# Kernel tuning notes

Measured on AMD Instinct MI355X. Metric: run time of the kernel, lower is better.

The kernel has to match this reference:

```python
import jax, jax.numpy as jnp
import numpy as np

N = 20000   # nodes
E = 320000  # edges
F = 64      # input node features
H = 256     # hidden_layer_size
C = 10      # nbr_classes
G = 64      # graphs in the batch


def _lin(key, fan_in, fan_out):
    k1, k2 = jax.random.split(key)
    bound = 1.0 / np.sqrt(fan_in)
    W = jax.random.uniform(k1, (fan_in, fan_out), jnp.float32, -bound, bound)
    b = jax.random.uniform(k2, (fan_out,), jnp.float32, -bound, bound)
    return W, b


def setup_inputs() -> dict:
    key = jax.random.key(0)
    ks = jax.random.split(key, 10)
    x = jax.random.normal(ks[0], (N, F), jnp.float32)
    edge_index = jax.random.randint(ks[1], (2, E), 0, N)
    batch = jnp.sort(jax.random.randint(ks[2], (N,), 0, G))
    W1, b1 = _lin(ks[3], F, H)
    W2, b2 = _lin(ks[4], H, H)
    W3, b3 = _lin(ks[5], H, H)
    W4, b4 = _lin(ks[6], H, H)
    W5, b5 = _lin(ks[7], H, H)
    Wout, bout = _lin(ks[8], H, C)
    return {"x": x, "edge_index": edge_index, "batch": batch,
            "W1": W1, "b1": b1, "W2": W2, "b2": b2, "W3": W3, "b3": b3,
            "W4": W4, "b4": b4, "W5": W5, "b5": b5, "Wout": Wout, "bout": bout}


def reference(x, edge_index, batch, W1, b1, W2, b2, W3, b3, W4, b4, W5, b5, Wout, bout):
    # GCNConv (Kipf & Welling): add self-loops, D^{-1/2}(A+I)D^{-1/2} (X W) + b.
    # Dropout(p=0.5) is identity in eval mode (reference is deterministic).
    loop = jnp.arange(N)
    row = jnp.concatenate([edge_index[0], loop])  # source nodes, [E+N]
    col = jnp.concatenate([edge_index[1], loop])  # target nodes, [E+N]
    deg = jax.ops.segment_sum(jnp.ones(E + N, x.dtype), col, num_segments=N)
    dinv = jax.lax.rsqrt(deg)  # deg >= 1 thanks to self-loops
    norm = (dinv[row] * dinv[col])[:, None]  # [E+N, 1]

    def gcn_conv(h, W, b):
        m = (h @ W)[row] * norm                      # gather + normalize, [E+N, H]
        return jax.ops.segment_sum(m, col, num_segments=N) + b

    h = x
    for W, b in ((W1, b1), (W2, b2), (W3, b3), (W4, b4), (W5, b5)):
        h = jax.nn.relu(gcn_conv(h, W, b))

    # global_mean_pool over graph ids
    counts = jax.ops.segment_sum(jnp.ones(N, h.dtype), batch, num_segments=G)
    pooled = jax.ops.segment_sum(h, batch, num_segments=G) / jnp.maximum(counts, 1.0)[:, None]
    return pooled @ Wout + bout  # [G, C]
```

## Files before the change

### kernel.cpp

```cpp
#include <hip/hip_runtime.h>

#define NN 20000
#define NE 320000
#define FIN 64
#define HD 256
#define NC 10
#define NG 64
#define NB ((NN + 255) / 256)

typedef unsigned short u16;
typedef unsigned int u32;
typedef __attribute__((ext_vector_type(8))) short short8;
typedef __attribute__((ext_vector_type(4))) float f32x4;

__device__ __forceinline__ float bf2f(u16 u) {
    union { u32 i; float f; } v; v.i = ((u32)u) << 16; return v.f;
}
__device__ __forceinline__ u16 f2bf(float f) {
    union { float f; u32 i; } v; v.f = f;
    u32 r = v.i + 0x7fffu + ((v.i >> 16) & 1u);
    return (u16)(r >> 16);
}

__global__ void k_prep(int* __restrict__ degi, int* __restrict__ gstart) {
    int i = blockIdx.x * 256 + threadIdx.x;
    if (i < NN) degi[i] = 0;
    if (i < NG) gstart[i] = NN;
}

__global__ void k_deg(const int* __restrict__ col, int* __restrict__ degi,
                      const int* __restrict__ batch, int* __restrict__ gstart) {
    int i = blockIdx.x * 256 + threadIdx.x;
    if (i < NE) atomicAdd(&degi[col[i]], 1);
    if (i < NN) {
        int b = batch[i];
        int prev = (i == 0) ? -1 : batch[i - 1];
        if (b != prev) gstart[b] = i;
    }
}

__global__ __launch_bounds__(256) void k_scan1(const int* __restrict__ degi,
                                               int* __restrict__ rowptr,
                                               int* __restrict__ bsum) {
    int t = threadIdx.x;
    int i = blockIdx.x * 256 + t;
    int v = (i < NN) ? degi[i] : 0;
    int lane = t & 63, wid = t >> 6;
    int x = v;
#pragma unroll
    for (int off = 1; off < 64; off <<= 1) {
        int y = __shfl_up(x, off);
        if (lane >= off) x += y;
    }
    __shared__ int ws[4];
    if (lane == 63) ws[wid] = x;
    __syncthreads();
    int woff = 0;
    for (int w = 0; w < wid; ++w) woff += ws[w];
    if (i < NN) rowptr[i] = woff + x - v;
    if (t == 255) bsum[blockIdx.x] = woff + x;
}

__global__ __launch_bounds__(128) void k_scan2(int* __restrict__ bsum, int* __restrict__ rowptr) {
    __shared__ int s[NB + 1];
    int t = threadIdx.x;
    if (t < NB) s[t] = bsum[t];
    __syncthreads();
    if (t == 0) {
        int run = 0;
        for (int k = 0; k < NB; ++k) { int tmp = s[k]; s[k] = run; run += tmp; }
        s[NB] = run;
    }
    __syncthreads();
    if (t < NB) bsum[t] = s[t];
    if (t == 0) rowptr[NN] = s[NB];
}

__global__ void k_scan3(const int* __restrict__ degi, const int* __restrict__ bsum,
                        int* __restrict__ rowptr, int* __restrict__ cursor,
                        float* __restrict__ dinv,
                        const float* __restrict__ x, u16* __restrict__ u0) {
    int i = blockIdx.x * 256 + threadIdx.x;
    if (i < NN) {
        int rp = rowptr[i] + bsum[i >> 8];
        rowptr[i] = rp;
        cursor[i] = rp;
        dinv[i] = rsqrtf((float)(1 + degi[i]));
    }
    if (i < NN * FIN / 4) {
        int node = i >> 4;
        float d = rsqrtf((float)(1 + degi[node]));
        float4 v = *(const float4*)&x[(size_t)i * 4];
        u32 lo = (u32)f2bf(v.x * d) | ((u32)f2bf(v.y * d) << 16);
        u32 hi = (u32)f2bf(v.z * d) | ((u32)f2bf(v.w * d) << 16);
        *(uint2*)&u0[(size_t)i * 4] = make_uint2(lo, hi);
    }
}

__global__ void k_fill(const int* __restrict__ row, const int* __restrict__ col,
                       int* __restrict__ cursor, int* __restrict__ ebuf) {
    int e = blockIdx.x * 256 + threadIdx.x;
    if (e < NE) {
        int c = col[e];
        int pos = atomicAdd(&cursor[c], 1);
        ebuf[pos] = row[e];
    }
}

__global__ __launch_bounds__(256) void k_trans(const float* __restrict__ W0, const float* __restrict__ W1,
                                               const float* __restrict__ W2, const float* __restrict__ W3,
                                               const float* __restrict__ W4,
                                               u16* __restrict__ T0, u16* __restrict__ T1,
                                               u16* __restrict__ T2, u16* __restrict__ T3,
                                               u16* __restrict__ T4) {
    int l = blockIdx.z;
    const float* W = (l == 0) ? W0 : (l == 1) ? W1 : (l == 2) ? W2 : (l == 3) ? W3 : W4;
    u16* T = (l == 0) ? T0 : (l == 1) ? T1 : (l == 2) ? T2 : (l == 3) ? T3 : T4;
    int K = (l == 0) ? FIN : HD;
    int k0 = blockIdx.x * 32;
    if (k0 >= K) return;
    int n0 = blockIdx.y * 32;
    __shared__ float tile[32][33];
    int tx = threadIdx.x & 31, ty = threadIdx.x >> 5;
#pragma unroll
    for (int r = 0; r < 32; r += 8)
        tile[ty + r][tx] = W[(size_t)(k0 + ty + r) * HD + n0 + tx];
    __syncthreads();
#pragma unroll
    for (int r = 0; r < 32; r += 8)
        T[(size_t)(n0 + ty + r) * K + k0 + tx] = f2bf(tile[tx][ty + r]);
}

__global__ __launch_bounds__(256) void k_gather256(const u16* __restrict__ U,
                                                   const int* __restrict__ rowptr,
                                                   const int* __restrict__ ebuf,
                                                   const float* __restrict__ dinv,
                                                   u16* __restrict__ Z) {
    int n = blockIdx.x * 4 + (threadIdx.x >> 6);
    if (n >= NN) return;
    int lane = threadIdx.x & 63;
    int half = lane >> 5;
    int seg = lane & 31;
    int s = rowptr[n], e = rowptr[n + 1];
    float acc[8];
    if (half == 0) {
        uint4 v = *(const uint4*)&U[(size_t)n * HD + seg * 8];
        acc[0] = bf2f((u16)(v.x & 0xffff)); acc[1] = bf2f((u16)(v.x >> 16));
        acc[2] = bf2f((u16)(v.y & 0xffff)); acc[3] = bf2f((u16)(v.y >> 16));
        acc[4] = bf2f((u16)(v.z & 0xffff)); acc[5] = bf2f((u16)(v.z >> 16));
        acc[6] = bf2f((u16)(v.w & 0xffff)); acc[7] = bf2f((u16)(v.w >> 16));
    } else {
#pragma unroll
        for (int k = 0; k < 8; ++k) acc[k] = 0.f;
    }
    for (int j = s; j < e; j += 32) {
        int idx = j + lane;
        int myid = (lane < 32 && idx < e) ? ebuf[idx] : -1;
        uint4 v[16];
#pragma unroll
        for (int k = 0; k < 16; ++k) {
            int r = __shfl(myid, 2 * k + half);
            uint4 t = *(const uint4*)&U[(size_t)max(r, 0) * HD + seg * 8];
            if (r < 0) t = make_uint4(0u, 0u, 0u, 0u);
            v[k] = t;
        }
#pragma unroll
        for (int k = 0; k < 16; ++k) {
            acc[0] += bf2f((u16)(v[k].x & 0xffff)); acc[1] += bf2f((u16)(v[k].x >> 16));
            acc[2] += bf2f((u16)(v[k].y & 0xffff)); acc[3] += bf2f((u16)(v[k].y >> 16));
            acc[4] += bf2f((u16)(v[k].z & 0xffff)); acc[5] += bf2f((u16)(v[k].z >> 16));
            acc[6] += bf2f((u16)(v[k].w & 0xffff)); acc[7] += bf2f((u16)(v[k].w >> 16));
        }
    }
#pragma unroll
    for (int k = 0; k < 8; ++k) acc[k] += __shfl_xor(acc[k], 32);
    if (half == 0) {
        float d = dinv[n];
        uint4 o;
        o.x = (u32)f2bf(acc[0] * d) | ((u32)f2bf(acc[1] * d) << 16);
        o.y = (u32)f2bf(acc[2] * d) | ((u32)f2bf(acc[3] * d) << 16);
        o.z = (u32)f2bf(acc[4] * d) | ((u32)f2bf(acc[5] * d) << 16);
        o.w = (u32)f2bf(acc[6] * d) | ((u32)f2bf(acc[7] * d) << 16);
        *(uint4*)&Z[(size_t)n * HD + seg * 8] = o;
    }
}

__global__ __launch_bounds__(256) void k_gather64(const u16* __restrict__ U,
                                                  const int* __restrict__ rowptr,
                                                  const int* __restrict__ ebuf,
                                                  const float* __restrict__ dinv,
                                                  u16* __restrict__ Z) {
    int n = blockIdx.x * 4 + (threadIdx.x >> 6);
    if (n >= NN) return;
    int lane = threadIdx.x & 63;
    int grp = lane >> 3;
    int seg = lane & 7;
    int s = rowptr[n], e = rowptr[n + 1];
    float acc[8];
    if (grp == 0) {
        uint4 v = *(const uint4*)&U[(size_t)n * FIN + seg * 8];
        acc[0] = bf2f((u16)(v.x & 0xffff)); acc[1] = bf2f((u16)(v.x >> 16));
        acc[2] = bf2f((u16)(v.y & 0xffff)); acc[3] = bf2f((u16)(v.y >> 16));
        acc[4] = bf2f((u16)(v.z & 0xffff)); acc[5] = bf2f((u16)(v.z >> 16));
        acc[6] = bf2f((u16)(v.w & 0xffff)); acc[7] = bf2f((u16)(v.w >> 16));
    } else {
#pragma unroll
        for (int k = 0; k < 8; ++k) acc[k] = 0.f;
    }
    for (int j = s; j < e; j += 16) {
        int i0 = j + grp, i1 = j + 8 + grp;
        int r0 = (i0 < e) ? ebuf[i0] : -1;
        int r1 = (i1 < e) ? ebuf[i1] : -1;
        uint4 v0 = *(const uint4*)&U[(size_t)max(r0, 0) * FIN + seg * 8];
        uint4 v1 = *(const uint4*)&U[(size_t)max(r1, 0) * FIN + seg * 8];
        if (r0 < 0) v0 = make_uint4(0u, 0u, 0u, 0u);
        if (r1 < 0) v1 = make_uint4(0u, 0u, 0u, 0u);
        acc[0] += bf2f((u16)(v0.x & 0xffff)); acc[1] += bf2f((u16)(v0.x >> 16));
        acc[2] += bf2f((u16)(v0.y & 0xffff)); acc[3] += bf2f((u16)(v0.y >> 16));
        acc[4] += bf2f((u16)(v0.z & 0xffff)); acc[5] += bf2f((u16)(v0.z >> 16));
        acc[6] += bf2f((u16)(v0.w & 0xffff)); acc[7] += bf2f((u16)(v0.w >> 16));
        acc[0] += bf2f((u16)(v1.x & 0xffff)); acc[1] += bf2f((u16)(v1.x >> 16));
        acc[2] += bf2f((u16)(v1.y & 0xffff)); acc[3] += bf2f((u16)(v1.y >> 16));
        acc[4] += bf2f((u16)(v1.z & 0xffff)); acc[5] += bf2f((u16)(v1.z >> 16));
        acc[6] += bf2f((u16)(v1.w & 0xffff)); acc[7] += bf2f((u16)(v1.w >> 16));
    }
#pragma unroll
    for (int off = 8; off < 64; off <<= 1)
#pragma unroll
        for (int k = 0; k < 8; ++k) acc[k] += __shfl_xor(acc[k], off);
    if (grp == 0) {
        float d = dinv[n];
        uint4 o;
        o.x = (u32)f2bf(acc[0] * d) | ((u32)f2bf(acc[1] * d) << 16);
        o.y = (u32)f2bf(acc[2] * d) | ((u32)f2bf(acc[3] * d) << 16);
        o.z = (u32)f2bf(acc[4] * d) | ((u32)f2bf(acc[5] * d) << 16);
        o.w = (u32)f2bf(acc[6] * d) | ((u32)f2bf(acc[7] * d) << 16);
        *(uint4*)&Z[(size_t)n * FIN + seg * 8] = o;
    }
}

__global__ __launch_bounds__(256) void k_mm(const u16* __restrict__ A,
                                            const u16* __restrict__ Wt,
                                            const float* __restrict__ bias,
                                            const float* __restrict__ dinv,
                                            u16* __restrict__ O,
                                            int K, int scaleOut) {
    __shared__ u16 Asm[64][40];
    __shared__ u16 Bsm[256][40];
    __shared__ float bs[HD];
    const int m0 = blockIdx.x * 64;
    const int t = threadIdx.x;
    const int wave = t >> 6;
    const int lane = t & 63;
    const int quad = lane >> 4;
    const int l16 = lane & 15;
    const int n0 = wave * 64;
    bs[t] = bias[t];

    f32x4 acc[4][4];
#pragma unroll
    for (int i = 0; i < 4; ++i)
#pragma unroll
        for (int j = 0; j < 4; ++j) acc[i][j] = (f32x4){0.f, 0.f, 0.f, 0.f};

    for (int k0 = 0; k0 < K; k0 += 32) {
        {
            int row = t >> 2, seg = t & 3;
            int gm = m0 + row;
            float4 v = make_float4(0.f, 0.f, 0.f, 0.f);
            if (gm < NN) v = *(const float4*)&A[(size_t)gm * K + k0 + seg * 8];
            *(float4*)&Asm[row][seg * 8] = v;
        }
        {
#pragma unroll
            for (int j = 0; j < 4; ++j) {
                float4 v = *(const float4*)&Wt[(size_t)t * K + k0 + j * 8];
                *(float4*)&Bsm[t][j * 8] = v;
            }
        }
        __syncthreads();
        short8 a[4], b[4];
#pragma unroll
        for (int i = 0; i < 4; ++i) a[i] = *(const short8*)&Asm[i * 16 + l16][quad * 8];
#pragma unroll
        for (int j = 0; j < 4; ++j) b[j] = *(const short8*)&Bsm[n0 + j * 16 + l16][quad * 8];
#pragma unroll
        for (int i = 0; i < 4; ++i)
#pragma unroll
            for (int j = 0; j < 4; ++j)
                acc[i][j] = __builtin_amdgcn_mfma_f32_16x16x32_bf16(a[i], b[j], acc[i][j], 0, 0, 0);
        __syncthreads();
    }
#pragma unroll
    for (int i = 0; i < 4; ++i) {
#pragma unroll
        for (int r = 0; r < 4; ++r) {
            int m = m0 + i * 16 + quad * 4 + r;
            if (m >= NN) continue;
            float d = scaleOut ? dinv[m] : 1.0f;
#pragma unroll
            for (int j = 0; j < 4; ++j) {
                int n = n0 + j * 16 + l16;
                float val = fmaxf(acc[i][j][r] + bs[n], 0.f) * d;
                O[(size_t)m * HD + n] = f2bf(val);
            }
        }
    }
}

__global__ __launch_bounds__(256) void k_poolout(const u16* __restrict__ h,
                                                 const int* __restrict__ gstart,
                                                 const float* __restrict__ Wout,
                                                 const float* __restrict__ bout,
                                                 float* __restrict__ out) {
    int g = blockIdx.x;
    int t = threadIdx.x;
    __shared__ float pooled[HD];
    __shared__ float part[NC][16];
    __shared__ int s_se[2];
    if (t == 0) {
        int st = gstart[g];
        int en = NN;
        for (int gg = g + 1; gg < NG; ++gg) en = min(en, gstart[gg]);
        s_se[0] = st; s_se[1] = en;
    }
    __syncthreads();
    int st = s_se[0], en = s_se[1];
    float a0 = 0.f, a1 = 0.f, a2 = 0.f, a3 = 0.f;
    int n = st;
    for (; n + 4 <= en; n += 4) {
        a0 += bf2f(h[(size_t)n * HD + t]);
        a1 += bf2f(h[(size_t)(n + 1) * HD + t]);
        a2 += bf2f(h[(size_t)(n + 2) * HD + t]);
        a3 += bf2f(h[(size_t)(n + 3) * HD + t]);
    }
    for (; n < en; ++n) a0 += bf2f(h[(size_t)n * HD + t]);
    float inv = 1.0f / (float)max(en - st, 1);
    pooled[t] = (a0 + a1 + a2 + a3) * inv;
    __syncthreads();
    if (t < NC * 16) {
        int c = t >> 4, l16 = t & 15;
        float s = 0.f;
        for (int f = l16; f < HD; f += 16)
            s = fmaf(pooled[f], Wout[(size_t)f * NC + c], s);
        part[c][l16] = s;
    }
    __syncthreads();
    if (t < NC) {
        float s = 0.f;
#pragma unroll
        for (int k = 0; k < 16; ++k) s += part[t][k];
        out[(size_t)g * NC + t] = s + bout[t];
    }
}

extern "C" void kernel_launch(void* const* d_in, const int* in_sizes, int n_in,
                              void* d_out, int out_size, void* d_ws, size_t ws_size,
                              hipStream_t stream) {
    const float* x     = (const float*)d_in[0];
    const int*   ei    = (const int*)d_in[1];
    const int*   batch = (const int*)d_in[2];
    const float* Wl[5] = {(const float*)d_in[3], (const float*)d_in[5], (const float*)d_in[7],
                          (const float*)d_in[9], (const float*)d_in[11]};
    const float* bl[5] = {(const float*)d_in[4], (const float*)d_in[6], (const float*)d_in[8],
                          (const float*)d_in[10], (const float*)d_in[12]};
    const float* Wout = (const float*)d_in[13];
    const float* bout = (const float*)d_in[14];
    float* out = (float*)d_out;

    const int* row = ei;
    const int* col = ei + NE;

    char* p = (char*)d_ws;
    auto take = [&](size_t bytes) { char* q = p; p += (bytes + 255) & ~(size_t)255; return q; };
    float* dinv   = (float*)take(NN * 4);
    int*   degi   = (int*)take(NN * 4);
    int*   rowptr = (int*)take((NN + 1) * 4);
    int*   cursor = (int*)take(NN * 4);
    int*   bsum   = (int*)take(NB * 4);
    int*   ebuf   = (int*)take(NE * 4);
    int*   gstart = (int*)take(NG * 4);
    u16*   Wt[5];
    for (int l = 0; l < 5; ++l) Wt[l] = (u16*)take((size_t)HD * HD * 2);
    u16*   B1     = (u16*)take((size_t)NN * HD * 2);
    u16*   B2     = (u16*)take((size_t)NN * HD * 2);

    k_prep<<<NB, 256, 0, stream>>>(degi, gstart);
    k_deg<<<(NE + 255) / 256, 256, 0, stream>>>(col, degi, batch, gstart);
    k_scan1<<<NB, 256, 0, stream>>>(degi, rowptr, bsum);
    k_scan2<<<1, 128, 0, stream>>>(bsum, rowptr);
    k_scan3<<<(NN * FIN / 4 + 255) / 256, 256, 0, stream>>>(degi, bsum, rowptr, cursor, dinv, x, B1);
    k_fill<<<(NE + 255) / 256, 256, 0, stream>>>(row, col, cursor, ebuf);
    dim3 tGrid(8, 8, 5);
    k_trans<<<tGrid, 256, 0, stream>>>(Wl[0], Wl[1], Wl[2], Wl[3], Wl[4],
                                       Wt[0], Wt[1], Wt[2], Wt[3], Wt[4]);

    k_gather64<<<(NN + 3) / 4, 256, 0, stream>>>(B1, rowptr, ebuf, dinv, B2);
    k_mm<<<(NN + 63) / 64, 256, 0, stream>>>(B2, Wt[0], bl[0], dinv, B1, FIN, 1);
    for (int l = 1; l < 5; ++l) {
        k_gather256<<<(NN + 3) / 4, 256, 0, stream>>>(B1, rowptr, ebuf, dinv, B2);
        k_mm<<<(NN + 63) / 64, 256, 0, stream>>>(B2, Wt[l], bl[l], dinv, B1, HD, (l < 4) ? 1 : 0);
    }

    k_poolout<<<NG, 256, 0, stream>>>(B1, gstart, Wout, bout, out);
}
```

Before: 351.8 us.

## Fuse neighbor gather and dense matmul into one kernel per GCN layer

Each GCN layer now runs as a single kernel. A block of 64 nodes first aggregates its neighbor rows into a shared-memory tile, then multiplies that tile by the transposed weights with MFMA. This removes the intermediate aggregated buffer's global write and read and halves the kernel launches. The cost is a much smaller grid (313 blocks instead of 5000) and each wave processing 16 nodes serially, which lowers latency hiding in the gather phase. Shared memory use also rises, which may reduce occupancy.

```diff
diff --git a/kernel.cpp b/kernel.cpp
--- a/kernel.cpp
+++ b/kernel.cpp
@@ -131,164 +131,103 @@
         T[(size_t)(n0 + ty + r) * K + k0 + tx] = f2bf(tile[tx][ty + r]);
 }
 
-__global__ __launch_bounds__(256) void k_gather256(const u16* __restrict__ U,
-                                                   const int* __restrict__ rowptr,
-                                                   const int* __restrict__ ebuf,
-                                                   const float* __restrict__ dinv,
-                                                   u16* __restrict__ Z) {
-    int n = blockIdx.x * 4 + (threadIdx.x >> 6);
-    if (n >= NN) return;
-    int lane = threadIdx.x & 63;
-    int half = lane >> 5;
-    int seg = lane & 31;
-    int s = rowptr[n], e = rowptr[n + 1];
-    float acc[8];
-    if (half == 0) {
-        uint4 v = *(const uint4*)&U[(size_t)n * HD + seg * 8];
-        acc[0] = bf2f((u16)(v.x & 0xffff)); acc[1] = bf2f((u16)(v.x >> 16));
-        acc[2] = bf2f((u16)(v.y & 0xffff)); acc[3] = bf2f((u16)(v.y >> 16));
-        acc[4] = bf2f((u16)(v.z & 0xffff)); acc[5] = bf2f((u16)(v.z >> 16));
-        acc[6] = bf2f((u16)(v.w & 0xffff)); acc[7] = bf2f((u16)(v.w >> 16));
-    } else {
-#pragma unroll
-        for (int k = 0; k < 8; ++k) acc[k] = 0.f;
-    }
-    for (int j = s; j < e; j += 32) {
-        int idx = j + lane;
-        int myid = (lane < 32 && idx < e) ? ebuf[idx] : -1;
-        uint4 v[16];
-#pragma unroll
-        for (int k = 0; k < 16; ++k) {
-            int r = __shfl(myid, 2 * k + half);
-            uint4 t = *(const uint4*)&U[(size_t)max(r, 0) * HD + seg * 8];
-            if (r < 0) t = make_uint4(0u, 0u, 0u, 0u);
-            v[k] = t;
-        }
-#pragma unroll
-        for (int k = 0; k < 16; ++k) {
-            acc[0] += bf2f((u16)(v[k].x & 0xffff)); acc[1] += bf2f((u16)(v[k].x >> 16));
-            acc[2] += bf2f((u16)(v[k].y & 0xffff)); acc[3] += bf2f((u16)(v[k].y >> 16));
-            acc[4] += bf2f((u16)(v[k].z & 0xffff)); acc[5] += bf2f((u16)(v[k].z >> 16));
-            acc[6] += bf2f((u16)(v[k].w & 0xffff)); acc[7] += bf2f((u16)(v[k].w >> 16));
-        }
-    }
-#pragma unroll
-    for (int k = 0; k < 8; ++k) acc[k] += __shfl_xor(acc[k], 32);
-    if (half == 0) {
-        float d = dinv[n];
-        uint4 o;
-        o.x = (u32)f2bf(acc[0] * d) | ((u32)f2bf(acc[1] * d) << 16);
-        o.y = (u32)f2bf(acc[2] * d) | ((u32)f2bf(acc[3] * d) << 16);
-        o.z = (u32)f2bf(acc[4] * d) | ((u32)f2bf(acc[5] * d) << 16);
-        o.w = (u32)f2bf(acc[6] * d) | ((u32)f2bf(acc[7] * d) << 16);
-        *(uint4*)&Z[(size_t)n * HD + seg * 8] = o;
-    }
-}
-
-__global__ __launch_bounds__(256) void k_gather64(const u16* __restrict__ U,
+__global__ __launch_bounds__(256) void k_layer256(const u16* __restrict__ U,
                                                   const int* __restrict__ rowptr,
                                                   const int* __restrict__ ebuf,
                                                   const float* __restrict__ dinv,
-                                                  u16* __restrict__ Z) {
-    int n = blockIdx.x * 4 + (threadIdx.x >> 6);
-    if (n >= NN) return;
-    int lane = threadIdx.x & 63;
-    int grp = lane >> 3;
-    int seg = lane & 7;
-    int s = rowptr[n], e = rowptr[n + 1];
-    float acc[8];
-    if (grp == 0) {
-        uint4 v = *(const uint4*)&U[(size_t)n * FIN + seg * 8];
-        acc[0] = bf2f((u16)(v.x & 0xffff)); acc[1] = bf2f((u16)(v.x >> 16));
-        acc[2] = bf2f((u16)(v.y & 0xffff)); acc[3] = bf2f((u16)(v.y >> 16));
-        acc[4] = bf2f((u16)(v.z & 0xffff)); acc[5] = bf2f((u16)(v.z >> 16));
-        acc[6] = bf2f((u16)(v.w & 0xffff)); acc[7] = bf2f((u16)(v.w >> 16));
-    } else {
-#pragma unroll
-        for (int k = 0; k < 8; ++k) acc[k] = 0.f;
-    }
-    for (int j = s; j < e; j += 16) {
-        int i0 = j + grp, i1 = j + 8 + grp;
-        int r0 = (i0 < e) ? ebuf[i0] : -1;
-        int r1 = (i1 < e) ? ebuf[i1] : -1;
-        uint4 v0 = *(const uint4*)&U[(size_t)max(r0, 0) * FIN + seg * 8];
-        uint4 v1 = *(const uint4*)&U[(size_t)max(r1, 0) * FIN + seg * 8];
-        if (r0 < 0) v0 = make_uint4(0u, 0u, 0u, 0u);
-        if (r1 < 0) v1 = make_uint4(0u, 0u, 0u, 0u);
-        acc[0] += bf2f((u16)(v0.x & 0xffff)); acc[1] += bf2f((u16)(v0.x >> 16));
-        acc[2] += bf2f((u16)(v0.y & 0xffff)); acc[3] += bf2f((u16)(v0.y >> 16));
-        acc[4] += bf2f((u16)(v0.z & 0xffff)); acc[5] += bf2f((u16)(v0.z >> 16));
-        acc[6] += bf2f((u16)(v0.w & 0xffff)); acc[7] += bf2f((u16)(v0.w >> 16));
-        acc[0] += bf2f((u16)(v1.x & 0xffff)); acc[1] += bf2f((u16)(v1.x >> 16));
-        acc[2] += bf2f((u16)(v1.y & 0xffff)); acc[3] += bf2f((u16)(v1.y >> 16));
-        acc[4] += bf2f((u16)(v1.z & 0xffff)); acc[5] += bf2f((u16)(v1.z >> 16));
-        acc[6] += bf2f((u16)(v1.w & 0xffff)); acc[7] += bf2f((u16)(v1.w >> 16));
-    }
-#pragma unroll
-    for (int off = 8; off < 64; off <<= 1)
-#pragma unroll
-        for (int k = 0; k < 8; ++k) acc[k] += __shfl_xor(acc[k], off);
-    if (grp == 0) {
-        float d = dinv[n];
-        uint4 o;
-        o.x = (u32)f2bf(acc[0] * d) | ((u32)f2bf(acc[1] * d) << 16);
-        o.y = (u32)f2bf(acc[2] * d) | ((u32)f2bf(acc[3] * d) << 16);
-        o.z = (u32)f2bf(acc[4] * d) | ((u32)f2bf(acc[5] * d) << 16);
-        o.w = (u32)f2bf(acc[6] * d) | ((u32)f2bf(acc[7] * d) << 16);
-        *(uint4*)&Z[(size_t)n * FIN + seg * 8] = o;
-    }
-}
-
-__global__ __launch_bounds__(256) void k_mm(const u16* __restrict__ A,
-                                            const u16* __restrict__ Wt,
-                                            const float* __restrict__ bias,
-                                            const float* __restrict__ dinv,
-                                            u16* __restrict__ O,
-                                            int K, int scaleOut) {
-    __shared__ u16 Asm[64][40];
+                                                  const u16* __restrict__ Wt,
+                                                  const float* __restrict__ bias,
+                                                  u16* __restrict__ O,
+                                                  int scaleOut) {
+    __shared__ u16 Zsm[64][264];
     __shared__ u16 Bsm[256][40];
     __shared__ float bs[HD];
     const int m0 = blockIdx.x * 64;
     const int t = threadIdx.x;
     const int wave = t >> 6;
     const int lane = t & 63;
+    bs[t] = bias[t];
+
+    const int half = lane >> 5;
+    const int seg = lane & 31;
+    for (int ni = 0; ni < 16; ++ni) {
+        int zrow = wave * 16 + ni;
+        int n = m0 + zrow;
+        if (n < NN) {
+            int s = rowptr[n], e = rowptr[n + 1];
+            float acc[8];
+            if (half == 0) {
+                uint4 v = *(const uint4*)&U[(size_t)n * HD + seg * 8];
+                acc[0] = bf2f((u16)(v.x & 0xffff)); acc[1] = bf2f((u16)(v.x >> 16));
+                acc[2] = bf2f((u16)(v.y & 0xffff)); acc[3] = bf2f((u16)(v.y >> 16));
+                acc[4] = bf2f((u16)(v.z & 0xffff)); acc[5] = bf2f((u16)(v.z >> 16));
+                acc[6] = bf2f((u16)(v.w & 0xffff)); acc[7] = bf2f((u16)(v.w >> 16));
+            } else {
+#pragma unroll
+                for (int k = 0; k < 8; ++k) acc[k] = 0.f;
+            }
+            for (int j = s; j < e; j += 32) {
+                int idx = j + lane;
+                int myid = (lane < 32 && idx < e) ? ebuf[idx] : -1;
+                uint4 v[16];
+#pragma unroll
+                for (int k = 0; k < 16; ++k) {
+                    int r = __shfl(myid, 2 * k + half);
+                    uint4 tv = *(const uint4*)&U[(size_t)max(r, 0) * HD + seg * 8];
+                    if (r < 0) tv = make_uint4(0u, 0u, 0u, 0u);
+                    v[k] = tv;
+                }
+#pragma unroll
+                for (int k = 0; k < 16; ++k) {
+                    acc[0] += bf2f((u16)(v[k].x & 0xffff)); acc[1] += bf2f((u16)(v[k].x >> 16));
+                    acc[2] += bf2f((u16)(v[k].y & 0xffff)); acc[3] += bf2f((u16)(v[k].y >> 16));
+                    acc[4] += bf2f((u16)(v[k].z & 0xffff)); acc[5] += bf2f((u16)(v[k].z >> 16));
+                    acc[6] += bf2f((u16)(v[k].w & 0xffff)); acc[7] += bf2f((u16)(v[k].w >> 16));
+                }
+            }
+#pragma unroll
+            for (int k = 0; k < 8; ++k) acc[k] += __shfl_xor(acc[k], 32);
+            if (half == 0) {
+                float d = dinv[n];
+                uint4 o;
+                o.x = (u32)f2bf(acc[0] * d) | ((u32)f2bf(acc[1] * d) << 16);
+                o.y = (u32)f2bf(acc[2] * d) | ((u32)f2bf(acc[3] * d) << 16);
+                o.z = (u32)f2bf(acc[4] * d) | ((u32)f2bf(acc[5] * d) << 16);
+                o.w = (u32)f2bf(acc[6] * d) | ((u32)f2bf(acc[7] * d) << 16);
+                *(uint4*)&Zsm[zrow][seg * 8] = o;
+            }
+        } else if (half == 0) {
+            *(uint4*)&Zsm[zrow][seg * 8] = make_uint4(0u, 0u, 0u, 0u);
+        }
+    }
+    __syncthreads();
+
     const int quad = lane >> 4;
     const int l16 = lane & 15;
     const int n0 = wave * 64;
-    bs[t] = bias[t];
-
-    f32x4 acc[4][4];
+    f32x4 acc2[4][4];
 #pragma unroll
     for (int i = 0; i < 4; ++i)
 #pragma unroll
-        for (int j = 0; j < 4; ++j) acc[i][j] = (f32x4){0.f, 0.f, 0.f, 0.f};
-
-    for (int k0 = 0; k0 < K; k0 += 32) {
-        {
-            int row = t >> 2, seg = t & 3;
-            int gm = m0 + row;
-            float4 v = make_float4(0.f, 0.f, 0.f, 0.f);
-            if (gm < NN) v = *(const float4*)&A[(size_t)gm * K + k0 + seg * 8];
-            *(float4*)&Asm[row][seg * 8] = v;
-        }
-        {
-#pragma unroll
-            for (int j = 0; j < 4; ++j) {
-                float4 v = *(const float4*)&Wt[(size_t)t * K + k0 + j * 8];
-                *(float4*)&Bsm[t][j * 8] = v;
-            }
+        for (int j = 0; j < 4; ++j) acc2[i][j] = (f32x4){0.f, 0.f, 0.f, 0.f};
+
+    for (int k0 = 0; k0 < HD; k0 += 32) {
+#pragma unroll
+        for (int j = 0; j < 4; ++j) {
+            float4 v = *(const float4*)&Wt[(size_t)t * HD + k0 + j * 8];
+            *(float4*)&Bsm[t][j * 8] = v;
         }
         __syncthreads();
         short8 a[4], b[4];
 #pragma unroll
-        for (int i = 0; i < 4; ++i) a[i] = *(const short8*)&Asm[i * 16 + l16][quad * 8];
+        for (int i = 0; i < 4; ++i) a[i] = *(const short8*)&Zsm[i * 16 + l16][k0 + quad * 8];
 #pragma unroll
         for (int j = 0; j < 4; ++j) b[j] = *(const short8*)&Bsm[n0 + j * 16 + l16][quad * 8];
 #pragma unroll
         for (int i = 0; i < 4; ++i)
 #pragma unroll
             for (int j = 0; j < 4; ++j)
-                acc[i][j] = __builtin_amdgcn_mfma_f32_16x16x32_bf16(a[i], b[j], acc[i][j], 0, 0, 0);
+                acc2[i][j] = __builtin_amdgcn_mfma_f32_16x16x32_bf16(a[i], b[j], acc2[i][j], 0, 0, 0);
         __syncthreads();
     }
 #pragma unroll
@@ -301,7 +240,118 @@
 #pragma unroll
             for (int j = 0; j < 4; ++j) {
                 int n = n0 + j * 16 + l16;
-                float val = fmaxf(acc[i][j][r] + bs[n], 0.f) * d;
+                float val = fmaxf(acc2[i][j][r] + bs[n], 0.f) * d;
+                O[(size_t)m * HD + n] = f2bf(val);
+            }
+        }
+    }
+}
+
+__global__ __launch_bounds__(256) void k_layer64(const u16* __restrict__ U,
+                                                 const int* __restrict__ rowptr,
+                                                 const int* __restrict__ ebuf,
+                                                 const float* __restrict__ dinv,
+                                                 const u16* __restrict__ Wt,
+                                                 const float* __restrict__ bias,
+                                                 u16* __restrict__ O) {
+    __shared__ u16 Zsm[64][72];
+    __shared__ u16 Bsm[256][72];
+    __shared__ float bs[HD];
+    const int m0 = blockIdx.x * 64;
+    const int t = threadIdx.x;
+    const int wave = t >> 6;
+    const int lane = t & 63;
+    bs[t] = bias[t];
+#pragma unroll
+    for (int j = 0; j < 8; ++j)
+        *(float4*)&Bsm[t][j * 8] = *(const float4*)&Wt[(size_t)t * FIN + j * 8];
+
+    const int grp = lane >> 3;
+    const int seg = lane & 7;
+    for (int ni = 0; ni < 16; ++ni) {
+        int zrow = wave * 16 + ni;
+        int n = m0 + zrow;
+        if (n < NN) {
+            int s = rowptr[n], e = rowptr[n + 1];
+            float acc[8];
+            if (grp == 0) {
+                uint4 v = *(const uint4*)&U[(size_t)n * FIN + seg * 8];
+                acc[0] = bf2f((u16)(v.x & 0xffff)); acc[1] = bf2f((u16)(v.x >> 16));
+                acc[2] = bf2f((u16)(v.y & 0xffff)); acc[3] = bf2f((u16)(v.y >> 16));
+                acc[4] = bf2f((u16)(v.z & 0xffff)); acc[5] = bf2f((u16)(v.z >> 16));
+                acc[6] = bf2f((u16)(v.w & 0xffff)); acc[7] = bf2f((u16)(v.w >> 16));
+            } else {
+#pragma unroll
+                for (int k = 0; k < 8; ++k) acc[k] = 0.f;
+            }
+            for (int j = s; j < e; j += 16) {
+                int i0 = j + grp, i1 = j + 8 + grp;
+                int r0 = (i0 < e) ? ebuf[i0] : -1;
+                int r1 = (i1 < e) ? ebuf[i1] : -1;
+                uint4 v0 = *(const uint4*)&U[(size_t)max(r0, 0) * FIN + seg * 8];
+                uint4 v1 = *(const uint4*)&U[(size_t)max(r1, 0) * FIN + seg * 8];
+                if (r0 < 0) v0 = make_uint4(0u, 0u, 0u, 0u);
+                if (r1 < 0) v1 = make_uint4(0u, 0u, 0u, 0u);
+                acc[0] += bf2f((u16)(v0.x & 0xffff)); acc[1] += bf2f((u16)(v0.x >> 16));
+                acc[2] += bf2f((u16)(v0.y & 0xffff)); acc[3] += bf2f((u16)(v0.y >> 16));
+                acc[4] += bf2f((u16)(v0.z & 0xffff)); acc[5] += bf2f((u16)(v0.z >> 16));
+                acc[6] += bf2f((u16)(v0.w & 0xffff)); acc[7] += bf2f((u16)(v0.w >> 16));
+                acc[0] += bf2f((u16)(v1.x & 0xffff)); acc[1] += bf2f((u16)(v1.x >> 16));
+                acc[2] += bf2f((u16)(v1.y & 0xffff)); acc[3] += bf2f((u16)(v1.y >> 16));
+                acc[4] += bf2f((u16)(v1.z & 0xffff)); acc[5] += bf2f((u16)(v1.z >> 16));
+                acc[6] += bf2f((u16)(v1.w & 0xffff)); acc[7] += bf2f((u16)(v1.w >> 16));
+            }
+#pragma unroll
+            for (int off = 8; off < 64; off <<= 1)
+#pragma unroll
+                for (int k = 0; k < 8; ++k) acc[k] += __shfl_xor(acc[k], off);
+            if (grp == 0) {
+                float d = dinv[n];
+                uint4 o;
+                o.x = (u32)f2bf(acc[0] * d) | ((u32)f2bf(acc[1] * d) << 16);
+                o.y = (u32)f2bf(acc[2] * d) | ((u32)f2bf(acc[3] * d) << 16);
+                o.z = (u32)f2bf(acc[4] * d) | ((u32)f2bf(acc[5] * d) << 16);
+                o.w = (u32)f2bf(acc[6] * d) | ((u32)f2bf(acc[7] * d) << 16);
+                *(uint4*)&Zsm[zrow][seg * 8] = o;
+            }
+        } else if (grp == 0) {
+            *(uint4*)&Zsm[zrow][seg * 8] = make_uint4(0u, 0u, 0u, 0u);
+        }
+    }
+    __syncthreads();
+
+    const int quad = lane >> 4;
+    const int l16 = lane & 15;
+    const int n0 = wave * 64;
+    f32x4 acc2[4][4];
+#pragma unroll
+    for (int i = 0; i < 4; ++i)
+#pragma unroll
+        for (int j = 0; j < 4; ++j) acc2[i][j] = (f32x4){0.f, 0.f, 0.f, 0.f};
+#pragma unroll
+    for (int k0 = 0; k0 < FIN; k0 += 32) {
+        short8 a[4], b[4];
+#pragma unroll
+        for (int i = 0; i < 4; ++i) a[i] = *(const short8*)&Zsm[i * 16 + l16][k0 + quad * 8];
+#pragma unroll
+        for (int j = 0; j < 4; ++j) b[j] = *(const short8*)&Bsm[n0 + j * 16 + l16][k0 + quad * 8];
+#pragma unroll
+        for (int i = 0; i < 4; ++i)
+#pragma unroll
+            for (int j = 0; j < 4; ++j)
+                acc2[i][j] = __builtin_amdgcn_mfma_f32_16x16x32_bf16(a[i], b[j], acc2[i][j], 0, 0, 0);
+    }
+#pragma unroll
+    for (int i = 0; i < 4; ++i) {
+#pragma unroll
+        for (int r = 0; r < 4; ++r) {
+            int m = m0 + i * 16 + quad * 4 + r;
+            if (m >= NN) continue;
+            float d = dinv[m];
+#pragma unroll
+            for (int j = 0; j < 4; ++j) {
+                int n = n0 + j * 16 + l16;
+                float val = fmaxf(acc2[i][j][r] + bs[n], 0.f) * d;
                 O[(size_t)m * HD + n] = f2bf(val);
             }
         }
@@ -395,12 +445,12 @@
     k_trans<<<tGrid, 256, 0, stream>>>(Wl[0], Wl[1], Wl[2], Wl[3], Wl[4],
                                        Wt[0], Wt[1], Wt[2], Wt[3], Wt[4]);
 
-    k_gather64<<<(NN + 3) / 4, 256, 0, stream>>>(B1, rowptr, ebuf, dinv, B2);
-    k_mm<<<(NN + 63) / 64, 256, 0, stream>>>(B2, Wt[0], bl[0], dinv, B1, FIN, 1);
-    for (int l = 1; l < 5; ++l) {
-        k_gather256<<<(NN + 3) / 4, 256, 0, stream>>>(B1, rowptr, ebuf, dinv, B2);
-        k_mm<<<(NN + 63) / 64, 256, 0, stream>>>(B2, Wt[l], bl[l], dinv, B1, HD, (l < 4) ? 1 : 0);
-    }
-
-    k_poolout<<<NG, 256, 0, stream>>>(B1, gstart, Wout, bout, out);
-}
+    const int grid = (NN + 63) / 64;
+    k_layer64<<<grid, 256, 0, stream>>>(B1, rowptr, ebuf, dinv, Wt[0], bl[0], B2);
+    k_layer256<<<grid, 256, 0, stream>>>(B2, rowptr, ebuf, dinv, Wt[1], bl[1], B1, 1);
+    k_layer256<<<grid, 256, 0, stream>>>(B1, rowptr, ebuf, dinv, Wt[2], bl[2], B2, 1);
+    k_layer256<<<grid, 256, 0, stream>>>(B2, rowptr, ebuf, dinv, Wt[3], bl[3], B1, 1);
+    k_layer256<<<grid, 256, 0, stream>>>(B1, rowptr, ebuf, dinv, Wt[4], bl[4], B2, 0);
+
+    k_poolout<<<NG, 256, 0, stream>>>(B2, gstart, Wout, bout, out);
+}
```

Result: slower. 413.5 us (+17.5%).

## Split hidden gather across feature halves; fold scan2 into scan3 and use memsets

Applied to the files above, without the earlier changes.

The 256-wide neighbour gather now splits each node's feature row across two blocks, each covering 128 features. Within a wave, four 16-lane groups each handle one edge, so a step walks 16 edges instead of 32 and ends with a two-stage shuffle reduction. With an average degree around 17, this should cut wasted masked loads on short rows and give more blocks for latency hiding, at the cost of fewer loads in flight per lane. Separately, the single-block scan2 kernel is removed: every scan3 block now redoes the small block-sum prefix in shared memory and writes the rowptr tail itself. The prep kernel is replaced by hipMemsetAsync calls, which changes the gstart sentinel from NN to 0x7F7F7F7F.

```diff
diff --git a/kernel.cpp b/kernel.cpp
--- a/kernel.cpp
+++ b/kernel.cpp
@@ -20,12 +20,6 @@
     union { float f; u32 i; } v; v.f = f;
     u32 r = v.i + 0x7fffu + ((v.i >> 16) & 1u);
     return (u16)(r >> 16);
-}
-
-__global__ void k_prep(int* __restrict__ degi, int* __restrict__ gstart) {
-    int i = blockIdx.x * 256 + threadIdx.x;
-    if (i < NN) degi[i] = 0;
-    if (i < NG) gstart[i] = NN;
 }
 
 __global__ void k_deg(const int* __restrict__ col, int* __restrict__ degi,
@@ -61,31 +55,26 @@
     if (t == 255) bsum[blockIdx.x] = woff + x;
 }
 
-__global__ __launch_bounds__(128) void k_scan2(int* __restrict__ bsum, int* __restrict__ rowptr) {
-    __shared__ int s[NB + 1];
-    int t = threadIdx.x;
-    if (t < NB) s[t] = bsum[t];
-    __syncthreads();
-    if (t == 0) {
-        int run = 0;
-        for (int k = 0; k < NB; ++k) { int tmp = s[k]; s[k] = run; run += tmp; }
-        s[NB] = run;
-    }
-    __syncthreads();
-    if (t < NB) bsum[t] = s[t];
-    if (t == 0) rowptr[NN] = s[NB];
-}
-
 __global__ void k_scan3(const int* __restrict__ degi, const int* __restrict__ bsum,
                         int* __restrict__ rowptr, int* __restrict__ cursor,
                         float* __restrict__ dinv,
                         const float* __restrict__ x, u16* __restrict__ u0) {
+    __shared__ int pref[NB];
+    if (threadIdx.x < NB) pref[threadIdx.x] = bsum[threadIdx.x];
+    __syncthreads();
+    if (threadIdx.x == 0) {
+        int run = 0;
+        for (int k = 0; k < NB; ++k) { int t = pref[k]; pref[k] = run; run += t; }
+    }
+    __syncthreads();
     int i = blockIdx.x * 256 + threadIdx.x;
     if (i < NN) {
-        int rp = rowptr[i] + bsum[i >> 8];
+        int dg = degi[i];
+        int rp = rowptr[i] + pref[i >> 8];
         rowptr[i] = rp;
         cursor[i] = rp;
-        dinv[i] = rsqrtf((float)(1 + degi[i]));
+        dinv[i] = rsqrtf((float)(1 + dg));
+        if (i == NN - 1) rowptr[NN] = rp + dg;
     }
     if (i < NN * FIN / 4) {
         int node = i >> 4;
@@ -131,20 +120,24 @@
         T[(size_t)(n0 + ty + r) * K + k0 + tx] = f2bf(tile[tx][ty + r]);
 }
 
-__global__ __launch_bounds__(256) void k_gather256(const u16* __restrict__ U,
-                                                   const int* __restrict__ rowptr,
-                                                   const int* __restrict__ ebuf,
-                                                   const float* __restrict__ dinv,
-                                                   u16* __restrict__ Z) {
-    int n = blockIdx.x * 4 + (threadIdx.x >> 6);
+__global__ __launch_bounds__(256) void k_gatherh(const u16* __restrict__ U,
+                                                 const int* __restrict__ rowptr,
+                                                 const int* __restrict__ ebuf,
+                                                 const float* __restrict__ dinv,
+                                                 u16* __restrict__ Z) {
+    int b = blockIdx.x;
+    int half = b & 1;
+    int tile = b >> 1;
+    int n = tile * 4 + (threadIdx.x >> 6);
     if (n >= NN) return;
     int lane = threadIdx.x & 63;
-    int half = lane >> 5;
-    int seg = lane & 31;
+    int grp = lane >> 4;
+    int seg = lane & 15;
+    int fbase = half * 128 + seg * 8;
     int s = rowptr[n], e = rowptr[n + 1];
     float acc[8];
-    if (half == 0) {
-        uint4 v = *(const uint4*)&U[(size_t)n * HD + seg * 8];
+    if (grp == 0) {
+        uint4 v = *(const uint4*)&U[(size_t)n * HD + fbase];
         acc[0] = bf2f((u16)(v.x & 0xffff)); acc[1] = bf2f((u16)(v.x >> 16));
         acc[2] = bf2f((u16)(v.y & 0xffff)); acc[3] = bf2f((u16)(v.y >> 16));
         acc[4] = bf2f((u16)(v.z & 0xffff)); acc[5] = bf2f((u16)(v.z >> 16));
@@ -153,19 +146,19 @@
 #pragma unroll
         for (int k = 0; k < 8; ++k) acc[k] = 0.f;
     }
-    for (int j = s; j < e; j += 32) {
+    for (int j = s; j < e; j += 16) {
         int idx = j + lane;
-        int myid = (lane < 32 && idx < e) ? ebuf[idx] : -1;
-        uint4 v[16];
-#pragma unroll
-        for (int k = 0; k < 16; ++k) {
-            int r = __shfl(myid, 2 * k + half);
-            uint4 t = *(const uint4*)&U[(size_t)max(r, 0) * HD + seg * 8];
+        int myid = (lane < 16 && idx < e) ? ebuf[idx] : -1;
+        uint4 v[4];
+#pragma unroll
+        for (int k = 0; k < 4; ++k) {
+            int r = __shfl(myid, grp * 4 + k);
+            uint4 t = *(const uint4*)&U[(size_t)max(r, 0) * HD + fbase];
             if (r < 0) t = make_uint4(0u, 0u, 0u, 0u);
             v[k] = t;
         }
 #pragma unroll
-        for (int k = 0; k < 16; ++k) {
+        for (int k = 0; k < 4; ++k) {
             acc[0] += bf2f((u16)(v[k].x & 0xffff)); acc[1] += bf2f((u16)(v[k].x >> 16));
             acc[2] += bf2f((u16)(v[k].y & 0xffff)); acc[3] += bf2f((u16)(v[k].y >> 16));
             acc[4] += bf2f((u16)(v[k].z & 0xffff)); acc[5] += bf2f((u16)(v[k].z >> 16));
@@ -173,15 +166,18 @@
         }
     }
 #pragma unroll
-    for (int k = 0; k < 8; ++k) acc[k] += __shfl_xor(acc[k], 32);
-    if (half == 0) {
+    for (int k = 0; k < 8; ++k) {
+        acc[k] += __shfl_xor(acc[k], 16);
+        acc[k] += __shfl_xor(acc[k], 32);
+    }
+    if (grp == 0) {
         float d = dinv[n];
         uint4 o;
         o.x = (u32)f2bf(acc[0] * d) | ((u32)f2bf(acc[1] * d) << 16);
         o.y = (u32)f2bf(acc[2] * d) | ((u32)f2bf(acc[3] * d) << 16);
         o.z = (u32)f2bf(acc[4] * d) | ((u32)f2bf(acc[5] * d) << 16);
         o.w = (u32)f2bf(acc[6] * d) | ((u32)f2bf(acc[7] * d) << 16);
-        *(uint4*)&Z[(size_t)n * HD + seg * 8] = o;
+        *(uint4*)&Z[(size_t)n * HD + fbase] = o;
     }
 }
 
@@ -385,10 +381,10 @@
     u16*   B1     = (u16*)take((size_t)NN * HD * 2);
     u16*   B2     = (u16*)take((size_t)NN * HD * 2);
 
-    k_prep<<<NB, 256, 0, stream>>>(degi, gstart);
+    hipMemsetAsync(degi, 0, NN * 4, stream);
+    hipMemsetAsync(gstart, 0x7F, NG * 4, stream);
     k_deg<<<(NE + 255) / 256, 256, 0, stream>>>(col, degi, batch, gstart);
     k_scan1<<<NB, 256, 0, stream>>>(degi, rowptr, bsum);
-    k_scan2<<<1, 128, 0, stream>>>(bsum, rowptr);
     k_scan3<<<(NN * FIN / 4 + 255) / 256, 256, 0, stream>>>(degi, bsum, rowptr, cursor, dinv, x, B1);
     k_fill<<<(NE + 255) / 256, 256, 0, stream>>>(row, col, cursor, ebuf);
     dim3 tGrid(8, 8, 5);
@@ -397,8 +393,9 @@
 
     k_gather64<<<(NN + 3) / 4, 256, 0, stream>>>(B1, rowptr, ebuf, dinv, B2);
     k_mm<<<(NN + 63) / 64, 256, 0, stream>>>(B2, Wt[0], bl[0], dinv, B1, FIN, 1);
+    const int gGrid = 2 * ((NN + 3) / 4);
     for (int l = 1; l < 5; ++l) {
-        k_gather256<<<(NN + 3) / 4, 256, 0, stream>>>(B1, rowptr, ebuf, dinv, B2);
+        k_gatherh<<<gGrid, 256, 0, stream>>>(B1, rowptr, ebuf, dinv, B2);
         k_mm<<<(NN + 63) / 64, 256, 0, stream>>>(B2, Wt[l], bl[l], dinv, B1, HD, (l < 4) ? 1 : 0);
     }
 
```

Result: no change. 350.4 us (-0.4%).
